# Performance work log

Measured on AMD Instinct MI355X. Metric: run time of the kernel, lower is better.

## Reference

```python
import jax, jax.numpy as jnp
import numpy as np


def setup_inputs() -> dict:
    key = jax.random.key(0)
    k1, k2, k3, k4 = jax.random.split(key, 4)
    B, K, UNITS, P, Q = 1024, 256, 32, 4, 4
    xavier = float(np.sqrt(6.0 / (K + K)))  # xavier_uniform bound for (k,k) fan
    inputs = jax.random.normal(k1, (B, K, P), dtype=jnp.float32)
    state = jax.random.normal(k2, (B, K * UNITS, Q), dtype=jnp.float32)
    kernel = jax.random.uniform(k3, (P, UNITS, K, K), dtype=jnp.float32, minval=-xavier, maxval=xavier)
    recurrent_kernel = jax.random.uniform(k4, (Q, UNITS, K, K), dtype=jnp.float32, minval=-xavier, maxval=xavier)
    return {"inputs": inputs, "state": state, "kernel": kernel, "recurrent_kernel": recurrent_kernel}


def reference(inputs, state, kernel, recurrent_kernel):
    # inputs: (B, k, p); state: (B, k*units, q)
    # kernel: (p, units, k, k); recurrent_kernel: (q, units, k, k)
    p, units, k, _ = kernel.shape
    q = recurrent_kernel.shape[0]
    B = inputs.shape[0]
    # AR part: sum_p (B,k) @ (units,k,k) -> (B, k_out, units), laid out k-major
    ar = jnp.einsum('bip,puij->bju', inputs, kernel).reshape(B, k * units)
    # MA part: state reshaped (B, k, units, q); per-lag per-unit (B,k)@(k,k)
    st = state.reshape(B, k, units, q)
    ma = jnp.einsum('biuq,quij->bju', st, recurrent_kernel).reshape(B, k * units)
    out = (ar + ma)[:, :, None]  # linear activation, (B, k*units, 1)
    out_state = jnp.concatenate([out, state[:, :, :-1]], axis=-1)  # (B, k*units, q)
    return out, out_state
```

## Files before the change

kernel.cpp:

```cpp
#include <hip/hip_runtime.h>
#include <hip/hip_bf16.h>


typedef __attribute__((ext_vector_type(8))) short bf16x8;
typedef __attribute__((ext_vector_type(4))) float f32x4;

__device__ inline unsigned short f2bf(float x) {
    unsigned int u = __float_as_uint(x);
    return (unsigned short)((u + 0x7fffu + ((u >> 16) & 1u)) >> 16);
}

__device__ inline void cvt_store4(unsigned short* dst, float4 v) {
    float2 ab; ab.x = v.x; ab.y = v.y;
    float2 cd; cd.x = v.z; cd.y = v.w;
    __hip_bfloat162 lo = __float22bfloat162_rn(ab);
    __hip_bfloat162 hi = __float22bfloat162_rn(cd);
    union { __hip_bfloat162 h2[2]; uint2 u2; } pk;
    pk.h2[0] = lo; pk.h2[1] = hi;
    *(uint2*)dst = pk.u2;
}

__device__ inline void cvt_store2(unsigned short* dst, float4 v) {
    float2 ab; ab.x = v.x; ab.y = v.y;
    float2 cd; cd.x = v.z; cd.y = v.w;
    __hip_bfloat162 lo = __float22bfloat162_rn(ab);
    __hip_bfloat162 hi = __float22bfloat162_rn(cd);
    union { __hip_bfloat162 h2[2]; uint2 u2; } pk;
    pk.h2[0] = lo; pk.h2[1] = hi;
    *(uint2*)dst = pk.u2;
}


__global__ __launch_bounds__(256) void prep_all(
    const float* __restrict__ kern,
    const float* __restrict__ rkern,
    const float* __restrict__ inputs,
    const float* __restrict__ state,
    unsigned short* __restrict__ Wtt,
    unsigned short* __restrict__ At_ar,
    unsigned short* __restrict__ At_ma)
{
    __shared__ char smem_raw[40960];
    const int bid = blockIdx.x;
    const int t = threadIdx.x;

    if (bid < 4096) {
        unsigned short* T = (unsigned short*)smem_raw;
        const int u  = bid & 31;
        const int jy = (bid >> 5) & 3;
        const int zz = bid >> 7;
        const int j0 = jy * 64;
        const int mm = zz >> 4;
        const int it = zz & 15;
        const float* src = mm ? rkern : kern;
        const int kout = mm * 1024 + it * 64;

        const int jq = t & 3;
        const int ii = (t >> 2) & 15;
        const int pp = t >> 6;
        const int i  = it * 16 + ii;
        const int kk = ii * 4 + pp;
        const float* row = src + ((size_t)((pp * 32 + u) * 256 + i)) * 256 + j0 + jq * 16;
        #pragma unroll
        for (int s = 0; s < 4; ++s) {
            float4 v = *(const float4*)(row + s * 4);
            const int jb_ = jq * 16 + s * 4;
            T[(jb_ + 0) * 72 + kk] = f2bf(v.x);
            T[(jb_ + 1) * 72 + kk] = f2bf(v.y);
            T[(jb_ + 2) * 72 + kk] = f2bf(v.z);
            T[(jb_ + 3) * 72 + kk] = f2bf(v.w);
        }
        __syncthreads();
        const int j = t >> 2, q = t & 3;
        const int kglob = kout + q * 16;
        const int kt  = kglob >> 5;
        const int kk0 = kglob & 31;
        const int jbo = jy >> 1;
        const int jloc = (jy & 1) * 64 + j;
        unsigned short* dst = Wtt +
            ((((size_t)(u * 2 + jbo) * 64 + kt) * 128 + jloc) * 32 + kk0);
        uint4 a = *(uint4*)&T[j * 72 + q * 16];
        uint4 b = *(uint4*)&T[j * 72 + q * 16 + 8];
        *(uint4*)dst = a;
        *(uint4*)(dst + 8) = b;
    } else if (bid < 4608) {
        const int b2 = bid - 4096;
        const size_t e = ((size_t)b2 * 256 + t) * 8;
        const int b = (int)(e >> 10), k = (int)(e & 1023);
        float4 v0 = *(const float4*)(inputs + e);
        float4 v1 = *(const float4*)(inputs + e + 4);
        const int mb = b >> 6, row = b & 63, kt = k >> 5, kk = k & 31;
        unsigned short* d = At_ar + (((size_t)(mb * 32 + kt) * 64 + row) * 32 + kk);
        cvt_store4(d, v0);
        cvt_store4(d + 4, v1);
    } else {
        unsigned short* L = (unsigned short*)smem_raw;
        const int b2  = bid - 4608;
        const int bt  = b2 & 63;
        const int ktp = b2 >> 6;

        const int r = t >> 4;
        const int l = t & 15;
        const float* src = state + (size_t)(bt * 16 + r) * 32768 + ktp * 1024 + l * 4;
        #pragma unroll
        for (int s = 0; s < 16; ++s) {
            float4 v = *(const float4*)(src + s * 64);
            const int c4   = l + s * 16;
            const int u    = c4 & 31;
            const int iloc = c4 >> 5;
            const int slot = iloc ^ (u & 7);
            cvt_store2(&L[(u * 16 + r) * 40 + slot * 4], v);
        }
        __syncthreads();
        const int mb   = bt >> 2;
        const int row0 = (bt & 3) * 16;
        const int part = t & 3;
        #pragma unroll
        for (int w = 0; w < 8; ++w) {
            const int pI = w * 64 + (t >> 2);
            const int u  = pI >> 4;
            const int rr = pI & 15;
            const int s0 = (2 * part) ^ (u & 7);
            const int s1 = (2 * part + 1) ^ (u & 7);
            uint2 d0 = *(const uint2*)&L[(u * 16 + rr) * 40 + s0 * 4];
            uint2 d1 = *(const uint2*)&L[(u * 16 + rr) * 40 + s1 * 4];
            uint4 o; o.x = d0.x; o.y = d0.y; o.z = d1.x; o.w = d1.y;
            unsigned short* dst = At_ma +
                ((((size_t)(u * 16 + mb) * 32 + ktp) * 64 + (row0 + rr)) * 32 + part * 8);
            *(uint4*)dst = o;
        }
    }
}

#define PITCH 40

__global__ __launch_bounds__(256, 4) void arma_gemm_mfma2ct(
    const unsigned short* __restrict__ At_ar,
    const unsigned short* __restrict__ At_ma,
    const unsigned short* __restrict__ Wtt,
    float* __restrict__ Ct)
{
    const int bid  = blockIdx.x;
    const int xcd  = bid & 7;
    const int slot = bid >> 3;
    const int pair = xcd * 8 + (slot & 7);
    const int mb   = slot >> 3;
    const int u    = pair >> 1;
    const int jb   = pair & 1;
    const int b0 = mb * 64;
    const int j0 = jb * 128;
    const int t  = threadIdx.x;
    const int lane = t & 63;
    const int wn = (t >> 6) * 32;
    const int fm = lane & 15;
    const int kq = lane >> 4;

    __shared__ unsigned short Asr[2][64 * PITCH];
    __shared__ unsigned short Wsr[2][128 * PITCH];

    const int ar_row = t >> 2, ar_off = (t & 3) * 8;
    const int w_row  = t >> 1, w_off  = (t & 1) * 16;

    f32x4 acc[4][2];
    #pragma unroll
    for (int a = 0; a < 4; ++a)
        #pragma unroll
        for (int b = 0; b < 2; ++b)
            acc[a][b] = (f32x4)0.0f;

    const unsigned short* abase_ar = At_ar + (size_t)mb * 32 * 2048 + t * 8;
    const unsigned short* abase_ma = At_ma + (size_t)(u * 16 + mb) * 32 * 2048 + t * 8;
    const unsigned short* wbase    = Wtt + (size_t)(u * 2 + jb) * 64 * 4096 + t * 16;

    uint4 av, w0, w1;

    auto LOADW = [&](int kt) {
        const unsigned short* tw = wbase + (size_t)kt * 4096;
        w0 = *(const uint4*)tw;
        w1 = *(const uint4*)(tw + 8);
    };
    auto STORE = [&](int buf) {
        *(uint4*)&Asr[buf][ar_row * PITCH + ar_off] = av;
        unsigned short* wd = &Wsr[buf][w_row * PITCH + w_off];
        *(uint4*)wd = w0;
        *(uint4*)(wd + 8) = w1;
    };
    auto COMPUTE = [&](int buf) {
        bf16x8 af[4], bfr[2];
        #pragma unroll
        for (int mt = 0; mt < 4; ++mt)
            af[mt] = *(const bf16x8*)&Asr[buf][(mt * 16 + fm) * PITCH + kq * 8];
        #pragma unroll
        for (int nt = 0; nt < 2; ++nt)
            bfr[nt] = *(const bf16x8*)&Wsr[buf][(wn + nt * 16 + fm) * PITCH + kq * 8];
        #pragma unroll
        for (int mt = 0; mt < 4; ++mt)
            #pragma unroll
            for (int nt = 0; nt < 2; ++nt)
                acc[mt][nt] = __builtin_amdgcn_mfma_f32_16x16x32_bf16(
                    af[mt], bfr[nt], acc[mt][nt], 0, 0, 0);
    };

    av = *(const uint4*)abase_ar;
    LOADW(0);
    STORE(0);
    __syncthreads();

    int cur = 0;
    for (int kt = 0; kt < 63; ++kt) {
        const int kn = kt + 1;
        const unsigned short* ta = (kn < 32) ? (abase_ar + (size_t)kn * 2048)
                                             : (abase_ma + (size_t)(kn - 32) * 2048);
        av = *(const uint4*)ta;
        LOADW(kn);
        COMPUTE(cur);
        STORE(cur ^ 1);
        __syncthreads();
        cur ^= 1;
    }
    COMPUTE(cur);

    #pragma unroll
    for (int mt = 0; mt < 4; ++mt) {
        const int rbase = b0 + mt * 16 + kq * 4;
        #pragma unroll
        for (int nt = 0; nt < 2; ++nt) {
            const int col = j0 + wn + nt * 16 + fm;
            float* op = Ct + (size_t)u * 262144 + (size_t)rbase * 256 + col;
            op[0]       = acc[mt][nt][0];
            op[256]     = acc[mt][nt][1];
            op[2 * 256] = acc[mt][nt][2];
            op[3 * 256] = acc[mt][nt][3];
        }
    }
}

__global__ __launch_bounds__(256) void arma_assemble3(
    const float* __restrict__ state,
    const float* __restrict__ Ct,
    float* __restrict__ out,
    float* __restrict__ out_state)
{
    const int b = blockIdx.x;
    const int t = threadIdx.x;
    __shared__ float L[256 * 33];
    for (int u = 0; u < 32; ++u)
        L[t * 33 + u] = Ct[((size_t)u * 1024 + b) * 256 + t];
    __syncthreads();
    const float* srow = state + (size_t)b * 32768;
    float* orow  = out + (size_t)b * 8192;
    float* osrow = out_state + (size_t)b * 32768;
    for (int w = 0; w < 32; ++w) {
        const int n = w * 256 + t;
        const float o = L[(n >> 5) * 33 + (n & 31)];
        const f32x4 s = *(const f32x4*)(srow + (size_t)n * 4);
        __builtin_nontemporal_store(o, orow + n);
        f32x4 rv = { o, s[0], s[1], s[2] };
        __builtin_nontemporal_store(rv, (f32x4*)(osrow + (size_t)n * 4));
    }
}

#define BM 64
#define BN 64
#define BKF 16
#define LDP 68

__global__ __launch_bounds__(256) void arma_gemm_f32(
    const float* __restrict__ inputs, const float* __restrict__ state,
    const float* __restrict__ kern, const float* __restrict__ rkern,
    float* __restrict__ out)
{
    const int u = blockIdx.z, b0 = blockIdx.x * BM, j0 = blockIdx.y * BN;
    const int tid = threadIdx.x;
    __shared__ float As[BKF][LDP];
    __shared__ float Ws[BKF][LDP];
    const int tx = tid & 15, ty = tid >> 4;
    const int arow = tid >> 2, ak4 = (tid & 3) * 4;
    const int wrow = tid >> 4, wj = (tid & 15) * 4;
    float acc[4][4] = {{0.f}};
    for (int kt = 0; kt < 1024; kt += BKF) {
        const float4 av = *(const float4*)(inputs + (size_t)(b0 + arow) * 1024 + kt + ak4);
        As[ak4 + 0][arow] = av.x; As[ak4 + 1][arow] = av.y;
        As[ak4 + 2][arow] = av.z; As[ak4 + 3][arow] = av.w;
        const int ip = kt + wrow;
        const float4 wv = *(const float4*)(kern + ((size_t)(((ip & 3) * 32 + u) * 256 + (ip >> 2))) * 256 + j0 + wj);
        *(float4*)&Ws[wrow][wj] = wv;
        __syncthreads();
        #pragma unroll
        for (int kk = 0; kk < BKF; ++kk) {
            const float4 a4 = *(const float4*)&As[kk][ty * 4];
            const float4 w4 = *(const float4*)&Ws[kk][tx * 4];
            acc[0][0] += a4.x * w4.x; acc[0][1] += a4.x * w4.y; acc[0][2] += a4.x * w4.z; acc[0][3] += a4.x * w4.w;
            acc[1][0] += a4.y * w4.x; acc[1][1] += a4.y * w4.y; acc[1][2] += a4.y * w4.z; acc[1][3] += a4.y * w4.w;
            acc[2][0] += a4.z * w4.x; acc[2][1] += a4.z * w4.y; acc[2][2] += a4.z * w4.z; acc[2][3] += a4.z * w4.w;
            acc[3][0] += a4.w * w4.x; acc[3][1] += a4.w * w4.y; acc[3][2] += a4.w * w4.z; acc[3][3] += a4.w * w4.w;
        }
        __syncthreads();
    }
    for (int kt = 0; kt < 1024; kt += BKF) {
        const int i = (kt >> 2) + (tid & 3);
        const float4 av = *(const float4*)(state + (size_t)(b0 + arow) * 32768 + (size_t)(i * 32 + u) * 4);
        As[ak4 + 0][arow] = av.x; As[ak4 + 1][arow] = av.y;
        As[ak4 + 2][arow] = av.z; As[ak4 + 3][arow] = av.w;
        const int iq = kt + wrow;
        const float4 wv = *(const float4*)(rkern + ((size_t)(((iq & 3) * 32 + u) * 256 + (iq >> 2))) * 256 + j0 + wj);
        *(float4*)&Ws[wrow][wj] = wv;
        __syncthreads();
        #pragma unroll
        for (int kk = 0; kk < BKF; ++kk) {
            const float4 a4 = *(const float4*)&As[kk][ty * 4];
            const float4 w4 = *(const float4*)&Ws[kk][tx * 4];
            acc[0][0] += a4.x * w4.x; acc[0][1] += a4.x * w4.y; acc[0][2] += a4.x * w4.z; acc[0][3] += a4.x * w4.w;
            acc[1][0] += a4.y * w4.x; acc[1][1] += a4.y * w4.y; acc[1][2] += a4.y * w4.z; acc[1][3] += a4.y * w4.w;
            acc[2][0] += a4.z * w4.x; acc[2][1] += a4.z * w4.y; acc[2][2] += a4.z * w4.z; acc[2][3] += a4.z * w4.w;
            acc[3][0] += a4.w * w4.x; acc[3][1] += a4.w * w4.y; acc[3][2] += a4.w * w4.z; acc[3][3] += a4.w * w4.w;
        }
        __syncthreads();
    }
    const int bb = b0 + ty * 4, jj = j0 + tx * 4;
    #pragma unroll
    for (int r = 0; r < 4; ++r)
        #pragma unroll
        for (int c = 0; c < 4; ++c)
            out[(size_t)(bb + r) * 8192 + (size_t)(jj + c) * 32 + u] = acc[r][c];
}

__global__ __launch_bounds__(256) void arma_assemble2(
    const float* __restrict__ state,
    const float* __restrict__ out,
    float* __restrict__ out_state)
{
    const size_t i = (size_t)blockIdx.x * 256 + threadIdx.x;
    const f32x4 o = *(const f32x4*)(out + i * 4);
    const float* sp = state + i * 16;
    const f32x4 s0 = *(const f32x4*)(sp + 0);
    const f32x4 s1 = *(const f32x4*)(sp + 4);
    const f32x4 s2 = *(const f32x4*)(sp + 8);
    const f32x4 s3 = *(const f32x4*)(sp + 12);
    f32x4 r0 = { o[0], s0[0], s0[1], s0[2] };
    f32x4 r1 = { o[1], s1[0], s1[1], s1[2] };
    f32x4 r2 = { o[2], s2[0], s2[1], s2[2] };
    f32x4 r3 = { o[3], s3[0], s3[1], s3[2] };
    f32x4* dp = (f32x4*)(out_state + i * 16);
    __builtin_nontemporal_store(r0, dp + 0);
    __builtin_nontemporal_store(r1, dp + 1);
    __builtin_nontemporal_store(r2, dp + 2);
    __builtin_nontemporal_store(r3, dp + 3);
}

extern "C" void kernel_launch(void* const* d_in, const int* in_sizes, int n_in,
                              void* d_out, int out_size, void* d_ws, size_t ws_size,
                              hipStream_t stream) {
    const float* inputs = (const float*)d_in[0];
    const float* state  = (const float*)d_in[1];
    const float* kern   = (const float*)d_in[2];
    const float* rkern  = (const float*)d_in[3];

    float* out       = (float*)d_out;
    float* out_state = (float*)d_out + 8388608;

    const size_t WTT_BYTES  = (size_t)32 * 2 * 64 * 128 * 32 * 2;
    const size_t ATAR_BYTES = (size_t)16 * 32 * 64 * 32 * 2;
    const size_t ATMA_BYTES = (size_t)32 * 16 * 32 * 64 * 32 * 2;
    const size_t CT_BYTES   = (size_t)32 * 1024 * 256 * 4;
    const size_t R3_BYTES   = WTT_BYTES + ATAR_BYTES + ATMA_BYTES + CT_BYTES;

    if (ws_size >= R3_BYTES) {
        unsigned short* Wtt   = (unsigned short*)d_ws;
        unsigned short* At_ar = (unsigned short*)((char*)d_ws + WTT_BYTES);
        unsigned short* At_ma = (unsigned short*)((char*)d_ws + WTT_BYTES + ATAR_BYTES);
        float* Ct             = (float*)((char*)d_ws + WTT_BYTES + ATAR_BYTES + ATMA_BYTES);
        prep_all<<<dim3(6656), 256, 0, stream>>>(kern, rkern, inputs, state,
                                                 Wtt, At_ar, At_ma);
        arma_gemm_mfma2ct<<<dim3(1024), 256, 0, stream>>>(At_ar, At_ma, Wtt, Ct);
        arma_assemble3<<<dim3(1024), 256, 0, stream>>>(state, Ct, out, out_state);
    } else {
        arma_gemm_f32<<<dim3(16, 4, 32), 256, 0, stream>>>(inputs, state, kern, rkern, out);
        arma_assemble2<<<8388608 / 4 / 256, 256, 0, stream>>>(state, out, out_state);
    }
}
```

Before: 425.9 us.

## Fuse state bf16 conversion into GEMM loads, drop At_ma prep pass

Removes the prep stage that transposed and converted the 128 MB fp32 state into a bf16 tiled buffer. The GEMM now reads fp32 state directly during the MA half of the K loop and converts it to bf16 while storing to shared memory. This saves a full write and reread of the intermediate buffer, but the GEMM now does strided fp32 loads from state (16-byte chunks at 512-byte stride) and bf16 conversion work inside the main loop.

Result: slower. 445.4 us (+4.6%).

```diff
diff --git a/kernel.cpp b/kernel.cpp
--- a/kernel.cpp
+++ b/kernel.cpp
@@ -35,17 +35,14 @@
     const float* __restrict__ kern,
     const float* __restrict__ rkern,
     const float* __restrict__ inputs,
-    const float* __restrict__ state,
     unsigned short* __restrict__ Wtt,
-    unsigned short* __restrict__ At_ar,
-    unsigned short* __restrict__ At_ma)
-{
-    __shared__ char smem_raw[40960];
+    unsigned short* __restrict__ At_ar)
+{
+    __shared__ unsigned short T[64 * 72];
     const int bid = blockIdx.x;
     const int t = threadIdx.x;
 
     if (bid < 4096) {
-        unsigned short* T = (unsigned short*)smem_raw;
         const int u  = bid & 31;
         const int jy = (bid >> 5) & 3;
         const int zz = bid >> 7;
@@ -83,7 +80,7 @@
         uint4 b = *(uint4*)&T[j * 72 + q * 16 + 8];
         *(uint4*)dst = a;
         *(uint4*)(dst + 8) = b;
-    } else if (bid < 4608) {
+    } else {
         const int b2 = bid - 4096;
         const size_t e = ((size_t)b2 * 256 + t) * 8;
         const int b = (int)(e >> 10), k = (int)(e & 1023);
@@ -93,50 +90,14 @@
         unsigned short* d = At_ar + (((size_t)(mb * 32 + kt) * 64 + row) * 32 + kk);
         cvt_store4(d, v0);
         cvt_store4(d + 4, v1);
-    } else {
-        unsigned short* L = (unsigned short*)smem_raw;
-        const int b2  = bid - 4608;
-        const int bt  = b2 & 63;
-        const int ktp = b2 >> 6;
-
-        const int r = t >> 4;
-        const int l = t & 15;
-        const float* src = state + (size_t)(bt * 16 + r) * 32768 + ktp * 1024 + l * 4;
-        #pragma unroll
-        for (int s = 0; s < 16; ++s) {
-            float4 v = *(const float4*)(src + s * 64);
-            const int c4   = l + s * 16;
-            const int u    = c4 & 31;
-            const int iloc = c4 >> 5;
-            const int slot = iloc ^ (u & 7);
-            cvt_store2(&L[(u * 16 + r) * 40 + slot * 4], v);
-        }
-        __syncthreads();
-        const int mb   = bt >> 2;
-        const int row0 = (bt & 3) * 16;
-        const int part = t & 3;
-        #pragma unroll
-        for (int w = 0; w < 8; ++w) {
-            const int pI = w * 64 + (t >> 2);
-            const int u  = pI >> 4;
-            const int rr = pI & 15;
-            const int s0 = (2 * part) ^ (u & 7);
-            const int s1 = (2 * part + 1) ^ (u & 7);
-            uint2 d0 = *(const uint2*)&L[(u * 16 + rr) * 40 + s0 * 4];
-            uint2 d1 = *(const uint2*)&L[(u * 16 + rr) * 40 + s1 * 4];
-            uint4 o; o.x = d0.x; o.y = d0.y; o.z = d1.x; o.w = d1.y;
-            unsigned short* dst = At_ma +
-                ((((size_t)(u * 16 + mb) * 32 + ktp) * 64 + (row0 + rr)) * 32 + part * 8);
-            *(uint4*)dst = o;
-        }
     }
 }
 
 #define PITCH 40
 
-__global__ __launch_bounds__(256, 4) void arma_gemm_mfma2ct(
+__global__ __launch_bounds__(256, 4) void arma_gemm_mfma3(
     const unsigned short* __restrict__ At_ar,
-    const unsigned short* __restrict__ At_ma,
+    const float* __restrict__ state,
     const unsigned short* __restrict__ Wtt,
     float* __restrict__ Ct)
 {
@@ -161,6 +122,9 @@
     const int ar_row = t >> 2, ar_off = (t & 3) * 8;
     const int w_row  = t >> 1, w_off  = (t & 1) * 16;
 
+    const int row0 = t >> 3,        ic0 = t & 7;
+    const int row1 = (t >> 3) + 32, ic1 = t & 7;
+
     f32x4 acc[4][2];
     #pragma unroll
     for (int a = 0; a < 4; ++a)
@@ -169,18 +133,27 @@
             acc[a][b] = (f32x4)0.0f;
 
     const unsigned short* abase_ar = At_ar + (size_t)mb * 32 * 2048 + t * 8;
-    const unsigned short* abase_ma = At_ma + (size_t)(u * 16 + mb) * 32 * 2048 + t * 8;
     const unsigned short* wbase    = Wtt + (size_t)(u * 2 + jb) * 64 * 4096 + t * 16;
+    const float* st0 = state + (size_t)(b0 + row0) * 32768 + u * 4 + ic0 * 128;
+    const float* st1 = state + (size_t)(b0 + row1) * 32768 + u * 4 + ic1 * 128;
 
     uint4 av, w0, w1;
+    float4 ma0, ma1;
 
     auto LOADW = [&](int kt) {
         const unsigned short* tw = wbase + (size_t)kt * 4096;
         w0 = *(const uint4*)tw;
         w1 = *(const uint4*)(tw + 8);
     };
-    auto STORE = [&](int buf) {
+    auto STORE_AR = [&](int buf) {
         *(uint4*)&Asr[buf][ar_row * PITCH + ar_off] = av;
+        unsigned short* wd = &Wsr[buf][w_row * PITCH + w_off];
+        *(uint4*)wd = w0;
+        *(uint4*)(wd + 8) = w1;
+    };
+    auto STORE_MA = [&](int buf) {
+        cvt_store2(&Asr[buf][row0 * PITCH + ic0 * 4], ma0);
+        cvt_store2(&Asr[buf][row1 * PITCH + ic1 * 4], ma1);
         unsigned short* wd = &Wsr[buf][w_row * PITCH + w_off];
         *(uint4*)wd = w0;
         *(uint4*)(wd + 8) = w1;
@@ -203,18 +176,25 @@
 
     av = *(const uint4*)abase_ar;
     LOADW(0);
-    STORE(0);
+    STORE_AR(0);
     __syncthreads();
 
     int cur = 0;
-    for (int kt = 0; kt < 63; ++kt) {
-        const int kn = kt + 1;
-        const unsigned short* ta = (kn < 32) ? (abase_ar + (size_t)kn * 2048)
-                                             : (abase_ma + (size_t)(kn - 32) * 2048);
-        av = *(const uint4*)ta;
-        LOADW(kn);
+    for (int kt = 0; kt < 31; ++kt) {
+        av = *(const uint4*)(abase_ar + (size_t)(kt + 1) * 2048);
+        LOADW(kt + 1);
         COMPUTE(cur);
-        STORE(cur ^ 1);
+        STORE_AR(cur ^ 1);
+        __syncthreads();
+        cur ^= 1;
+    }
+    for (int kt = 31; kt < 63; ++kt) {
+        const int ktp = kt + 1 - 32;
+        ma0 = *(const float4*)(st0 + (size_t)ktp * 1024);
+        ma1 = *(const float4*)(st1 + (size_t)ktp * 1024);
+        LOADW(kt + 1);
+        COMPUTE(cur);
+        STORE_MA(cur ^ 1);
         __syncthreads();
         cur ^= 1;
     }
@@ -361,18 +341,15 @@
 
     const size_t WTT_BYTES  = (size_t)32 * 2 * 64 * 128 * 32 * 2;
     const size_t ATAR_BYTES = (size_t)16 * 32 * 64 * 32 * 2;
-    const size_t ATMA_BYTES = (size_t)32 * 16 * 32 * 64 * 32 * 2;
     const size_t CT_BYTES   = (size_t)32 * 1024 * 256 * 4;
-    const size_t R3_BYTES   = WTT_BYTES + ATAR_BYTES + ATMA_BYTES + CT_BYTES;
-
-    if (ws_size >= R3_BYTES) {
+    const size_t R6_BYTES   = WTT_BYTES + ATAR_BYTES + CT_BYTES;
+
+    if (ws_size >= R6_BYTES) {
         unsigned short* Wtt   = (unsigned short*)d_ws;
         unsigned short* At_ar = (unsigned short*)((char*)d_ws + WTT_BYTES);
-        unsigned short* At_ma = (unsigned short*)((char*)d_ws + WTT_BYTES + ATAR_BYTES);
-        float* Ct             = (float*)((char*)d_ws + WTT_BYTES + ATAR_BYTES + ATMA_BYTES);
-        prep_all<<<dim3(6656), 256, 0, stream>>>(kern, rkern, inputs, state,
-                                                 Wtt, At_ar, At_ma);
-        arma_gemm_mfma2ct<<<dim3(1024), 256, 0, stream>>>(At_ar, At_ma, Wtt, Ct);
+        float* Ct             = (float*)((char*)d_ws + WTT_BYTES + ATAR_BYTES);
+        prep_all<<<dim3(4608), 256, 0, stream>>>(kern, rkern, inputs, Wtt, At_ar);
+        arma_gemm_mfma3<<<dim3(1024), 256, 0, stream>>>(At_ar, state, Wtt, Ct);
         arma_assemble3<<<dim3(1024), 256, 0, stream>>>(state, Ct, out, out_state);
     } else {
         arma_gemm_f32<<<dim3(16, 4, 32), 256, 0, stream>>>(inputs, state, kern, rkern, out);
```
